# Kernel optimization log

Hardware: AMD Instinct MI355X
Metric: run time of the kernel (lower is better)

The kernel has to match this reference:

```python
import math
import jax, jax.numpy as jnp
import numpy as np

HEADS = 8
DIM = 512
HEAD_SIZE = DIM // HEADS  # 64


def setup_inputs() -> dict:
    key = jax.random.key(0)
    ks = jax.random.split(key, 5)
    b, nh, nw, t, d = 16, 16, 16, 16, DIM
    x = jax.random.normal(ks[0], (b, nh, nw, t, d), dtype=jnp.float32)
    s = 1.0 / math.sqrt(d)
    Wq = jax.random.normal(ks[1], (d, d), dtype=jnp.float32) * s
    Wk = jax.random.normal(ks[2], (d, d), dtype=jnp.float32) * s
    Wv = jax.random.normal(ks[3], (d, d), dtype=jnp.float32) * s
    Wo = jax.random.normal(ks[4], (d, d), dtype=jnp.float32) * s
    z = jnp.zeros((d,), dtype=jnp.float32)
    return {"x": x, "Wq": Wq, "bq": z, "Wk": Wk, "bk": z, "Wv": Wv, "bv": z, "Wo": Wo, "bo": z}


def _split_heads(t):
    # [b, n1, n2, T, D] -> [b, n1, n2, H, T, hs]
    b, n1, n2, T, _ = t.shape
    return t.reshape(b, n1, n2, T, HEADS, HEAD_SIZE).transpose(0, 1, 2, 4, 3, 5)


def reference(x, Wq, bq, Wk, bk, Wv, bv, Wo, bo):
    q = _split_heads(x @ Wq + bq)
    k = _split_heads(x @ Wk + bk)
    v = _split_heads(x @ Wv + bv)
    # windowed attention scores: [b, n1, n2, H, T, T]
    scores = jnp.einsum('bnmhtd,bnmhsd->bnmhts', q, k) / math.sqrt(HEAD_SIZE)
    probs = jax.nn.sigmoid(scores)  # NOTE: elementwise sigmoid, not softmax
    ctx = jnp.einsum('bnmhts,bnmhsd->bnmhtd', probs, v)
    b, n1, n2, H, T, hs = ctx.shape
    ctx = ctx.transpose(0, 1, 2, 4, 3, 5).reshape(b, n1, n2, T, H * hs)
    return ctx @ Wo + bo
```

## Files before the change

kernel.cpp:

```cpp
#include <hip/hip_runtime.h>
#include <hip/hip_bf16.h>

typedef float f32x4 __attribute__((ext_vector_type(4)));
typedef __bf16 bf16x8 __attribute__((ext_vector_type(8)));
typedef unsigned short u16x4 __attribute__((ext_vector_type(4)));
typedef unsigned short u16x8 __attribute__((ext_vector_type(8)));

__device__ __forceinline__ unsigned short f2bf(float f) {
  union { float f; unsigned u; } x; x.f = f;
  unsigned r = x.u + 0x7FFFu + ((x.u >> 16) & 1u);
  return (unsigned short)(r >> 16);
}

__device__ __forceinline__ void gl16(const void* g, void* l) {
  __builtin_amdgcn_global_load_lds(
      (const __attribute__((address_space(1))) unsigned*)g,
      (__attribute__((address_space(3))) unsigned*)l, 16, 0, 0);
}

__global__ __launch_bounds__(256) void prep_wt(const float* __restrict__ Wq,
                                               const float* __restrict__ Wk,
                                               const float* __restrict__ Wv,
                                               const float* __restrict__ Wo,
                                               unsigned short* __restrict__ WT) {
  __shared__ unsigned short ts[64][65];
  const float* W = (blockIdx.z == 0) ? Wq : (blockIdx.z == 1) ? Wk
                   : (blockIdx.z == 2) ? Wv : Wo;
  const int t = threadIdx.x;
  const int kbase = blockIdx.y * 64;
  const int nbase = blockIdx.x * 64;
  for (int i = 0; i < 16; ++i) {
    int idx = i * 256 + t;
    int r = idx >> 6, c = idx & 63;
    ts[r][c] = f2bf(W[(size_t)(kbase + r) * 512 + nbase + c]);
  }
  __syncthreads();
  unsigned short* dst = WT + (size_t)blockIdx.z * 512 * 512;
  for (int i = 0; i < 16; ++i) {
    int idx = i * 256 + t;
    int nn = idx >> 6, kk = idx & 63;
    dst[(size_t)(nbase + nn) * 512 + kbase + kk] = ts[kk][nn];
  }
}

__global__ void prep_bias(const float* __restrict__ bq, const float* __restrict__ bk,
                          const float* __restrict__ bv, float* __restrict__ biasc) {
  int i = blockIdx.x * 256 + threadIdx.x;
  if (i < 512) biasc[i] = bq[i];
  else if (i < 1024) biasc[i] = bk[i - 512];
  else if (i < 1536) biasc[i] = bv[i - 1024];
}

__global__ __launch_bounds__(256) void convert_x(const float* __restrict__ x,
                                                 unsigned short* __restrict__ xb,
                                                 long long n8) {
  long long i = (long long)blockIdx.x * 256 + threadIdx.x;
  const long long stride = (long long)gridDim.x * 256;
  for (; i < n8; i += stride) {
    f32x4 a = *reinterpret_cast<const f32x4*>(&x[i * 8]);
    f32x4 b = *reinterpret_cast<const f32x4*>(&x[i * 8 + 4]);
    u16x8 o;
    o[0] = f2bf(a[0]); o[1] = f2bf(a[1]); o[2] = f2bf(a[2]); o[3] = f2bf(a[3]);
    o[4] = f2bf(b[0]); o[5] = f2bf(b[1]); o[6] = f2bf(b[2]); o[7] = f2bf(b[3]);
    *reinterpret_cast<u16x8*>(&xb[i * 8]) = o;
  }
}

template <typename CT>
__global__ __launch_bounds__(512, 2) void gemm256(
    const unsigned short* __restrict__ A, int lda,
    const unsigned short* __restrict__ BT,
    CT* __restrict__ C, int ldc,
    const float* __restrict__ bias, int NB) {
  __shared__ alignas(16) unsigned short pool[66048];
  const int t = threadIdx.x;
  const int lane = t & 63;
  const int w = t >> 6;
  const int wm = w >> 2, wn = w & 3;

  const int nwg = gridDim.x;
  const int cpx = nwg >> 3;
  const int wg = (blockIdx.x & 7) * cpx + (blockIdx.x >> 3);
  const int n0 = (wg % NB) * 256;
  const int m0 = (wg / NB) * 256;

  const int sr = lane >> 3;
  const int sg = ((lane & 7) ^ sr) << 3;
  const unsigned short* gA = A + (size_t)(m0 + w * 8 + sr) * lda + sg;
  const unsigned short* gB = BT + (size_t)(n0 + w * 8 + sr) * 512 + sg;
  const int lw = w * 512;

#define STAGE_A(kt, h, b)                                                   \
  { const unsigned short* g_ = gA + (size_t)(h) * 128 * lda + (kt) * 64;    \
    unsigned short* l_ = &pool[(b) * 16384 + (h) * 8192 + lw];              \
    gl16(g_, l_); gl16(g_ + (size_t)64 * lda, l_ + 4096); }
#define STAGE_B(kt, h, b)                                                   \
  { const unsigned short* g_ = gB + (size_t)(h) * 128 * 512 + (kt) * 64;    \
    unsigned short* l_ = &pool[32768 + (b) * 16384 + (h) * 8192 + lw];      \
    gl16(g_, l_); gl16(g_ + (size_t)64 * 512, l_ + 4096); }

  const int fr = lane & 15;
  const int fg = lane >> 4;
  const int fx = lane & 7;
  auto readA = [&](int b, int mi, int kf) -> bf16x8 {
    return *reinterpret_cast<const bf16x8*>(
        &pool[(b) * 16384 + (wm * 128 + mi * 16 + fr) * 64 +
              ((((kf << 2) + fg) ^ fx) << 3)]);
  };
  auto readB = [&](int b, int ni, int kf) -> bf16x8 {
    return *reinterpret_cast<const bf16x8*>(
        &pool[32768 + (b) * 16384 + (wn * 64 + ni * 16 + fr) * 64 +
              ((((kf << 2) + fg) ^ fx) << 3)]);
  };

  f32x4 acc[8][4];
#pragma unroll
  for (int i = 0; i < 8; ++i)
#pragma unroll
    for (int j = 0; j < 4; ++j) acc[i][j] = (f32x4){0.f, 0.f, 0.f, 0.f};
  bf16x8 afr[8];
  bf16x8 bfr[4][2];

#define PHASE2(b, h, READB, STAGES, VM)                                      \
  {                                                                          \
    afr[0] = readA(b, 4 * (h) + 0, 0); afr[1] = readA(b, 4 * (h) + 0, 1);    \
    afr[2] = readA(b, 4 * (h) + 1, 0); afr[3] = readA(b, 4 * (h) + 1, 1);    \
    afr[4] = readA(b, 4 * (h) + 2, 0); afr[5] = readA(b, 4 * (h) + 2, 1);    \
    afr[6] = readA(b, 4 * (h) + 3, 0); afr[7] = readA(b, 4 * (h) + 3, 1);    \
    if (READB) {                                                             \
      _Pragma("unroll") for (int ni = 0; ni < 4; ++ni) {                     \
        bfr[ni][0] = readB(b, ni, 0);                                        \
        bfr[ni][1] = readB(b, ni, 1);                                        \
      }                                                                      \
    }                                                                        \
    STAGES;                                                                  \
    if ((VM) == 4) asm volatile("s_waitcnt vmcnt(4)" ::: "memory");          \
    if ((VM) == 0) asm volatile("s_waitcnt vmcnt(0)" ::: "memory");          \
    __builtin_amdgcn_s_barrier();                                            \
    asm volatile("s_waitcnt lgkmcnt(0)" ::: "memory");                       \
    __builtin_amdgcn_sched_barrier(0);                                       \
    __builtin_amdgcn_s_setprio(1);                                           \
    _Pragma("unroll") for (int ni = 0; ni < 4; ++ni)                         \
      _Pragma("unroll") for (int m4 = 0; m4 < 4; ++m4)                       \
        acc[4 * (h) + m4][ni] = __builtin_amdgcn_mfma_f32_16x16x32_bf16(     \
            afr[2 * m4], bfr[ni][0], acc[4 * (h) + m4][ni], 0, 0, 0);        \
    _Pragma("unroll") for (int ni = 0; ni < 4; ++ni)                         \
      _Pragma("unroll") for (int m4 = 0; m4 < 4; ++m4)                       \
        acc[4 * (h) + m4][ni] = __builtin_amdgcn_mfma_f32_16x16x32_bf16(     \
            afr[2 * m4 + 1], bfr[ni][1], acc[4 * (h) + m4][ni], 0, 0, 0);    \
    __builtin_amdgcn_s_setprio(0);                                           \
    __builtin_amdgcn_s_barrier();                                            \
  }

  STAGE_B(0, 0, 0); STAGE_B(0, 1, 0);
  STAGE_A(0, 0, 0); STAGE_A(0, 1, 0);
  STAGE_B(1, 0, 1); STAGE_B(1, 1, 1);
  asm volatile("s_waitcnt vmcnt(4)" ::: "memory");
  __builtin_amdgcn_s_barrier();

#pragma unroll
  for (int i = 0; i < 4; ++i) {
    const bool s2 = (i < 3);
    PHASE2(0, 0, true,  { STAGE_A(2 * i + 1, 0, 1) STAGE_A(2 * i + 1, 1, 1) }, -1);
    PHASE2(0, 1, false, { if (s2) { STAGE_B(2 * i + 2, 0, 0) STAGE_B(2 * i + 2, 1, 0) } }, s2 ? 4 : 0);
    PHASE2(1, 0, true,  { if (s2) { STAGE_A(2 * i + 2, 0, 0) STAGE_A(2 * i + 2, 1, 0) } }, -1);
    PHASE2(1, 1, false, { if (s2) { STAGE_B(2 * i + 3, 0, 1) STAGE_B(2 * i + 3, 1, 1) } }, s2 ? 4 : 0);
  }
#undef PHASE2
#undef STAGE_A
#undef STAGE_B

  __syncthreads();
  if constexpr (sizeof(CT) == 2) {
#pragma unroll
    for (int ni = 0; ni < 4; ++ni) {
      int cl = wn * 64 + ni * 16 + fr;
      float bc = bias[n0 + cl];
#pragma unroll
      for (int mi = 0; mi < 8; ++mi) {
        int rl = wm * 128 + mi * 16 + fg * 4;
#pragma unroll
        for (int r = 0; r < 4; ++r)
          pool[(rl + r) * 258 + cl] = f2bf(acc[mi][ni][r] + bc);
      }
    }
    __syncthreads();
#pragma unroll
    for (int it = 0; it < 16; ++it) {
      int idx = it * 512 + t;
      int row = idx >> 5, c8 = idx & 31;
      u16x8 v = *reinterpret_cast<const u16x8*>(&pool[row * 258 + c8 * 8]);
      *reinterpret_cast<u16x8*>(&C[(size_t)(m0 + row) * ldc + n0 + c8 * 8]) = v;
    }
  } else {
    float* stf = reinterpret_cast<float*>(pool);
#pragma unroll
    for (int h = 0; h < 2; ++h) {
      if (wm == h) {
#pragma unroll
        for (int ni = 0; ni < 4; ++ni) {
          int cl = wn * 64 + ni * 16 + fr;
          float bc = bias[n0 + cl];
#pragma unroll
          for (int mi = 0; mi < 8; ++mi) {
            int rl = mi * 16 + fg * 4;
#pragma unroll
            for (int r = 0; r < 4; ++r)
              stf[(rl + r) * 258 + cl] = acc[mi][ni][r] + bc;
          }
        }
      }
      __syncthreads();
#pragma unroll
      for (int it = 0; it < 16; ++it) {
        int idx = it * 512 + t;
        int row = idx >> 6, c4 = idx & 63;
        f32x4 v = *reinterpret_cast<const f32x4*>(&stf[row * 258 + c4 * 4]);
        *reinterpret_cast<f32x4*>(
            &C[(size_t)(m0 + h * 128 + row) * ldc + n0 + c4 * 4]) = v;
      }
      __syncthreads();
    }
  }
}

__global__ __launch_bounds__(256) void attn2(unsigned short* __restrict__ QKV) {
  __shared__ alignas(16) unsigned short sh[33792];
  const int VS = 16384, PS = 32768;
  const int t = threadIdx.x;
  const int lane = t & 63;
  const int w = t >> 6;
  const int fr = lane & 15, fg = lane >> 4, fx = lane & 7;
  const int sr = lane >> 3;
  const int sgx = ((lane & 7) ^ sr) << 3;
  const int sgl = (lane & 7) << 3;
  const size_t m0r = (size_t)blockIdx.x * 128;

#define SK2(h, b)                                                            \
  _Pragma("unroll") for (int u = 0; u < 4; ++u) {                            \
    const int r0 = u * 32 + w * 8;                                           \
    gl16(QKV + (m0r + r0 + sr) * 1536 + 512 + (h) * 64 + sgx,                \
         &sh[(b) * 8192 + r0 * 64]);                                         \
  }
#define SV2(h, b)                                                            \
  _Pragma("unroll") for (int u = 0; u < 4; ++u) {                            \
    const int r0 = u * 32 + w * 8;                                           \
    gl16(QKV + (m0r + r0 + sr) * 1536 + 1024 + (h) * 64 + sgl,               \
         &sh[VS + (b) * 8192 + r0 * 64]);                                    \
  }

  SK2(0, 0) SV2(0, 0)
  asm volatile("s_waitcnt vmcnt(0)" ::: "memory");
  __syncthreads();

  for (int h = 0; h < 8; ++h) {
    const int b = h & 1;
    u16x8 q[2][2];
#pragma unroll
    for (int ww = 0; ww < 2; ++ww) {
      const int wi = w * 2 + ww;
      const unsigned short* qrow = QKV + (m0r + wi * 16 + fr) * 1536 + h * 64;
      q[ww][0] = *reinterpret_cast<const u16x8*>(qrow + fg * 8);
      q[ww][1] = *reinterpret_cast<const u16x8*>(qrow + 32 + fg * 8);
    }
    if (h < 7) { SK2(h + 1, b ^ 1) SV2(h + 1, b ^ 1) }

#pragma unroll
    for (int ww = 0; ww < 2; ++ww) {
      const int wi = w * 2 + ww;
      f32x4 s = (f32x4){0.f, 0.f, 0.f, 0.f};
      {
        bf16x8 kf_ = *reinterpret_cast<const bf16x8*>(
            &sh[b * 8192 + (wi * 16 + fr) * 64 + ((fg ^ fx) << 3)]);
        s = __builtin_amdgcn_mfma_f32_16x16x32_bf16(
            kf_, __builtin_bit_cast(bf16x8, q[ww][0]), s, 0, 0, 0);
        kf_ = *reinterpret_cast<const bf16x8*>(
            &sh[b * 8192 + (wi * 16 + fr) * 64 + (((4 + fg) ^ fx) << 3)]);
        s = __builtin_amdgcn_mfma_f32_16x16x32_bf16(
            kf_, __builtin_bit_cast(bf16x8, q[ww][1]), s, 0, 0, 0);
      }
      u16x4 pfu;
#pragma unroll
      for (int r = 0; r < 4; ++r)
        pfu[r] = f2bf(1.0f / (1.0f + __expf(-s[r] * 0.125f)));
      *reinterpret_cast<u16x4*>(&sh[PS + w * 256 + fr * 16 + fg * 4]) = pfu;
      u16x8 pbu = (u16x8){0, 0, 0, 0, 0, 0, 0, 0};
      if (fg < 2)
        pbu = *reinterpret_cast<const u16x8*>(&sh[PS + w * 256 + fr * 16 + fg * 8]);
      bf16x8 pb = __builtin_bit_cast(bf16x8, pbu);
#pragma unroll
      for (int dc = 0; dc < 4; ++dc) {
        u16x8 vau;
#pragma unroll
        for (int j = 0; j < 8; ++j)
          vau[j] = sh[VS + b * 8192 + (wi * 16 + (fg & 1) * 8 + j) * 64 + dc * 16 + fr];
        f32x4 c = __builtin_amdgcn_mfma_f32_16x16x32_bf16(
            __builtin_bit_cast(bf16x8, vau), pb, (f32x4){0.f, 0.f, 0.f, 0.f},
            0, 0, 0);
        u16x4 o;
#pragma unroll
        for (int r = 0; r < 4; ++r) o[r] = f2bf(c[r]);
        *reinterpret_cast<u16x4*>(
            &QKV[(m0r + wi * 16 + fr) * 1536 + 1024 + h * 64 + dc * 16 + fg * 4]) = o;
      }
    }
    asm volatile("s_waitcnt vmcnt(8)" ::: "memory");
    __syncthreads();
  }
#undef SK2
#undef SV2
}

extern "C" void kernel_launch(void* const* d_in, const int* in_sizes, int n_in,
                              void* d_out, int out_size, void* d_ws, size_t ws_size,
                              hipStream_t stream) {
  const float* x  = (const float*)d_in[0];
  const float* Wq = (const float*)d_in[1];
  const float* bq = (const float*)d_in[2];
  const float* Wk = (const float*)d_in[3];
  const float* bk = (const float*)d_in[4];
  const float* Wv = (const float*)d_in[5];
  const float* bv = (const float*)d_in[6];
  const float* Wo = (const float*)d_in[7];
  const float* bo = (const float*)d_in[8];
  float* out = (float*)d_out;

  const int M = 65536;
  char* ws = (char*)d_ws;
  unsigned short* WT = (unsigned short*)ws;
  float* biasc = (float*)(ws + (size_t)2048 * 512 * 2);
  const long long prep_bytes = (long long)2048 * 512 * 2 + 8192;

  prep_wt<<<dim3(8, 8, 4), 256, 0, stream>>>(Wq, Wk, Wv, Wo, WT);
  prep_bias<<<6, 256, 0, stream>>>(bq, bk, bv, biasc);

  long long avail = (long long)ws_size - prep_bytes;
  int chunk_rows = 65536;
  while (chunk_rows > 2048 && (long long)chunk_rows * 4096 > avail) chunk_rows >>= 1;
  const int nchunks = M / chunk_rows;

  unsigned short* Xb  = (unsigned short*)(ws + prep_bytes);
  unsigned short* QKV = Xb + (size_t)chunk_rows * 512;

  for (int c = 0; c < nchunks; ++c) {
    const size_t row0 = (size_t)c * chunk_rows;
    const int mt = chunk_rows / 256;
    convert_x<<<2048, 256, 0, stream>>>(x + row0 * 512, Xb,
                                        (long long)chunk_rows * 64);
    gemm256<unsigned short><<<mt * 6, 512, 0, stream>>>(
        Xb, 512, WT, QKV, 1536, biasc, 6);
    attn2<<<chunk_rows / 128, 256, 0, stream>>>(QKV);
    gemm256<float><<<mt * 2, 512, 0, stream>>>(
        QKV + 1024, 1536, WT + (size_t)1536 * 512, out + row0 * 512, 512, bo, 2);
  }
}
```

Baseline: 294.3 us.

## Replace 256x256 GEMM tile with simpler 128x128 double-buffered kernel

Swaps the hand-pipelined 256x256, 512-thread GEMM for a 128x128-tile, 256-thread kernel with BK=32 and a plain two-buffer prefetch loop. The new kernel uses far less LDS and targets four workgroups per CU. The goal is higher occupancy and more workgroups to balance across CUs. In exchange, each tile reuses data less, so global and L2 traffic per FLOP goes up, and the finely interleaved load/MFMA schedule is dropped.

```diff
diff --git a/kernel.cpp b/kernel.cpp
--- a/kernel.cpp
+++ b/kernel.cpp
@@ -67,129 +67,100 @@
 }
 
 template <typename CT>
-__global__ __launch_bounds__(512, 2) void gemm256(
+__global__ __launch_bounds__(256, 4) void gemm128(
     const unsigned short* __restrict__ A, int lda,
     const unsigned short* __restrict__ BT,
     CT* __restrict__ C, int ldc,
     const float* __restrict__ bias, int NB) {
-  __shared__ alignas(16) unsigned short pool[66048];
+  __shared__ alignas(16) unsigned short pool[16640];
   const int t = threadIdx.x;
   const int lane = t & 63;
   const int w = t >> 6;
-  const int wm = w >> 2, wn = w & 3;
+  const int wm = w >> 1, wn = w & 1;
 
   const int nwg = gridDim.x;
   const int cpx = nwg >> 3;
   const int wg = (blockIdx.x & 7) * cpx + (blockIdx.x >> 3);
-  const int n0 = (wg % NB) * 256;
-  const int m0 = (wg / NB) * 256;
-
-  const int sr = lane >> 3;
-  const int sg = ((lane & 7) ^ sr) << 3;
-  const unsigned short* gA = A + (size_t)(m0 + w * 8 + sr) * lda + sg;
-  const unsigned short* gB = BT + (size_t)(n0 + w * 8 + sr) * 512 + sg;
-  const int lw = w * 512;
-
-#define STAGE_A(kt, h, b)                                                   \
-  { const unsigned short* g_ = gA + (size_t)(h) * 128 * lda + (kt) * 64;    \
-    unsigned short* l_ = &pool[(b) * 16384 + (h) * 8192 + lw];              \
-    gl16(g_, l_); gl16(g_ + (size_t)64 * lda, l_ + 4096); }
-#define STAGE_B(kt, h, b)                                                   \
-  { const unsigned short* g_ = gB + (size_t)(h) * 128 * 512 + (kt) * 64;    \
-    unsigned short* l_ = &pool[32768 + (b) * 16384 + (h) * 8192 + lw];      \
-    gl16(g_, l_); gl16(g_ + (size_t)64 * 512, l_ + 4096); }
+  const int n0 = (wg % NB) * 128;
+  const int m0 = (wg / NB) * 128;
+
+  const int sgr = lane >> 2;
+  const int sgc = ((lane & 3) ^ ((lane >> 3) & 3)) << 3;
+  const unsigned short* gA = A + (size_t)(m0 + w * 32 + sgr) * lda + sgc;
+  const unsigned short* gB = BT + (size_t)(n0 + w * 32 + sgr) * 512 + sgc;
+  const int lw = w * 1024;
+
+#define SA(kt, b)                                                           \
+  { const unsigned short* g_ = gA + (kt) * 32;                              \
+    gl16(g_, &pool[(b) * 4096 + lw]);                                       \
+    gl16(g_ + (size_t)16 * lda, &pool[(b) * 4096 + lw + 512]); }
+#define SB(kt, b)                                                           \
+  { const unsigned short* g_ = gB + (kt) * 32;                              \
+    gl16(g_, &pool[8192 + (b) * 4096 + lw]);                                \
+    gl16(g_ + (size_t)16 * 512, &pool[8192 + (b) * 4096 + lw + 512]); }
 
   const int fr = lane & 15;
   const int fg = lane >> 4;
-  const int fx = lane & 7;
-  auto readA = [&](int b, int mi, int kf) -> bf16x8 {
-    return *reinterpret_cast<const bf16x8*>(
-        &pool[(b) * 16384 + (wm * 128 + mi * 16 + fr) * 64 +
-              ((((kf << 2) + fg) ^ fx) << 3)]);
-  };
-  auto readB = [&](int b, int ni, int kf) -> bf16x8 {
-    return *reinterpret_cast<const bf16x8*>(
-        &pool[32768 + (b) * 16384 + (wn * 64 + ni * 16 + fr) * 64 +
-              ((((kf << 2) + fg) ^ fx) << 3)]);
-  };
-
-  f32x4 acc[8][4];
-#pragma unroll
-  for (int i = 0; i < 8; ++i)
+  const int aslot = (fg ^ ((fr >> 1) & 3)) << 3;
+
+  f32x4 acc[4][4];
+#pragma unroll
+  for (int i = 0; i < 4; ++i)
 #pragma unroll
     for (int j = 0; j < 4; ++j) acc[i][j] = (f32x4){0.f, 0.f, 0.f, 0.f};
-  bf16x8 afr[8];
-  bf16x8 bfr[4][2];
-
-#define PHASE2(b, h, READB, STAGES, VM)                                      \
-  {                                                                          \
-    afr[0] = readA(b, 4 * (h) + 0, 0); afr[1] = readA(b, 4 * (h) + 0, 1);    \
-    afr[2] = readA(b, 4 * (h) + 1, 0); afr[3] = readA(b, 4 * (h) + 1, 1);    \
-    afr[4] = readA(b, 4 * (h) + 2, 0); afr[5] = readA(b, 4 * (h) + 2, 1);    \
-    afr[6] = readA(b, 4 * (h) + 3, 0); afr[7] = readA(b, 4 * (h) + 3, 1);    \
-    if (READB) {                                                             \
-      _Pragma("unroll") for (int ni = 0; ni < 4; ++ni) {                     \
-        bfr[ni][0] = readB(b, ni, 0);                                        \
-        bfr[ni][1] = readB(b, ni, 1);                                        \
-      }                                                                      \
-    }                                                                        \
-    STAGES;                                                                  \
-    if ((VM) == 4) asm volatile("s_waitcnt vmcnt(4)" ::: "memory");          \
-    if ((VM) == 0) asm volatile("s_waitcnt vmcnt(0)" ::: "memory");          \
-    __builtin_amdgcn_s_barrier();                                            \
-    asm volatile("s_waitcnt lgkmcnt(0)" ::: "memory");                       \
-    __builtin_amdgcn_sched_barrier(0);                                       \
-    __builtin_amdgcn_s_setprio(1);                                           \
-    _Pragma("unroll") for (int ni = 0; ni < 4; ++ni)                         \
-      _Pragma("unroll") for (int m4 = 0; m4 < 4; ++m4)                       \
-        acc[4 * (h) + m4][ni] = __builtin_amdgcn_mfma_f32_16x16x32_bf16(     \
-            afr[2 * m4], bfr[ni][0], acc[4 * (h) + m4][ni], 0, 0, 0);        \
-    _Pragma("unroll") for (int ni = 0; ni < 4; ++ni)                         \
-      _Pragma("unroll") for (int m4 = 0; m4 < 4; ++m4)                       \
-        acc[4 * (h) + m4][ni] = __builtin_amdgcn_mfma_f32_16x16x32_bf16(     \
-            afr[2 * m4 + 1], bfr[ni][1], acc[4 * (h) + m4][ni], 0, 0, 0);    \
-    __builtin_amdgcn_s_setprio(0);                                           \
-    __builtin_amdgcn_s_barrier();                                            \
-  }
-
-  STAGE_B(0, 0, 0); STAGE_B(0, 1, 0);
-  STAGE_A(0, 0, 0); STAGE_A(0, 1, 0);
-  STAGE_B(1, 0, 1); STAGE_B(1, 1, 1);
-  asm volatile("s_waitcnt vmcnt(4)" ::: "memory");
+  bf16x8 afr[4], bfr[4];
+
+  SA(0, 0) SB(0, 0)
+  asm volatile("s_waitcnt vmcnt(0)" ::: "memory");
   __builtin_amdgcn_s_barrier();
 
 #pragma unroll
-  for (int i = 0; i < 4; ++i) {
-    const bool s2 = (i < 3);
-    PHASE2(0, 0, true,  { STAGE_A(2 * i + 1, 0, 1) STAGE_A(2 * i + 1, 1, 1) }, -1);
-    PHASE2(0, 1, false, { if (s2) { STAGE_B(2 * i + 2, 0, 0) STAGE_B(2 * i + 2, 1, 0) } }, s2 ? 4 : 0);
-    PHASE2(1, 0, true,  { if (s2) { STAGE_A(2 * i + 2, 0, 0) STAGE_A(2 * i + 2, 1, 0) } }, -1);
-    PHASE2(1, 1, false, { if (s2) { STAGE_B(2 * i + 3, 0, 1) STAGE_B(2 * i + 3, 1, 1) } }, s2 ? 4 : 0);
-  }
-#undef PHASE2
-#undef STAGE_A
-#undef STAGE_B
-
-  __syncthreads();
+  for (int kt = 0; kt < 16; ++kt) {
+    const int b = kt & 1;
+    if (kt < 15) { SA(kt + 1, b ^ 1) SB(kt + 1, b ^ 1) }
+#pragma unroll
+    for (int mi = 0; mi < 4; ++mi)
+      afr[mi] = *reinterpret_cast<const bf16x8*>(
+          &pool[b * 4096 + (wm * 64 + mi * 16 + fr) * 32 + aslot]);
+#pragma unroll
+    for (int ni = 0; ni < 4; ++ni)
+      bfr[ni] = *reinterpret_cast<const bf16x8*>(
+          &pool[8192 + b * 4096 + (wn * 64 + ni * 16 + fr) * 32 + aslot]);
+    asm volatile("s_waitcnt lgkmcnt(0)" ::: "memory");
+    __builtin_amdgcn_sched_barrier(0);
+    __builtin_amdgcn_s_setprio(1);
+#pragma unroll
+    for (int mi = 0; mi < 4; ++mi)
+#pragma unroll
+      for (int ni = 0; ni < 4; ++ni)
+        acc[mi][ni] = __builtin_amdgcn_mfma_f32_16x16x32_bf16(
+            afr[mi], bfr[ni], acc[mi][ni], 0, 0, 0);
+    __builtin_amdgcn_s_setprio(0);
+    asm volatile("s_waitcnt vmcnt(0)" ::: "memory");
+    __builtin_amdgcn_s_barrier();
+  }
+#undef SA
+#undef SB
+
   if constexpr (sizeof(CT) == 2) {
 #pragma unroll
     for (int ni = 0; ni < 4; ++ni) {
       int cl = wn * 64 + ni * 16 + fr;
       float bc = bias[n0 + cl];
 #pragma unroll
-      for (int mi = 0; mi < 8; ++mi) {
-        int rl = wm * 128 + mi * 16 + fg * 4;
+      for (int mi = 0; mi < 4; ++mi) {
+        int rl = wm * 64 + mi * 16 + fg * 4;
 #pragma unroll
         for (int r = 0; r < 4; ++r)
-          pool[(rl + r) * 258 + cl] = f2bf(acc[mi][ni][r] + bc);
+          pool[(rl + r) * 130 + cl] = f2bf(acc[mi][ni][r] + bc);
       }
     }
     __syncthreads();
 #pragma unroll
-    for (int it = 0; it < 16; ++it) {
-      int idx = it * 512 + t;
-      int row = idx >> 5, c8 = idx & 31;
-      u16x8 v = *reinterpret_cast<const u16x8*>(&pool[row * 258 + c8 * 8]);
+    for (int it = 0; it < 8; ++it) {
+      int idx = it * 256 + t;
+      int row = idx >> 4, c8 = idx & 15;
+      u16x8 v = *reinterpret_cast<const u16x8*>(&pool[row * 130 + c8 * 8]);
       *reinterpret_cast<u16x8*>(&C[(size_t)(m0 + row) * ldc + n0 + c8 * 8]) = v;
     }
   } else {
@@ -202,22 +173,22 @@
           int cl = wn * 64 + ni * 16 + fr;
           float bc = bias[n0 + cl];
 #pragma unroll
-          for (int mi = 0; mi < 8; ++mi) {
+          for (int mi = 0; mi < 4; ++mi) {
             int rl = mi * 16 + fg * 4;
 #pragma unroll
             for (int r = 0; r < 4; ++r)
-              stf[(rl + r) * 258 + cl] = acc[mi][ni][r] + bc;
+              stf[(rl + r) * 130 + cl] = acc[mi][ni][r] + bc;
           }
         }
       }
       __syncthreads();
 #pragma unroll
-      for (int it = 0; it < 16; ++it) {
-        int idx = it * 512 + t;
-        int row = idx >> 6, c4 = idx & 63;
-        f32x4 v = *reinterpret_cast<const f32x4*>(&stf[row * 258 + c4 * 4]);
+      for (int it = 0; it < 8; ++it) {
+        int idx = it * 256 + t;
+        int row = idx >> 5, c4 = idx & 31;
+        f32x4 v = *reinterpret_cast<const f32x4*>(&stf[row * 130 + c4 * 4]);
         *reinterpret_cast<f32x4*>(
-            &C[(size_t)(m0 + h * 128 + row) * ldc + n0 + c4 * 4]) = v;
+            &C[(size_t)(m0 + h * 64 + row) * ldc + n0 + c4 * 4]) = v;
       }
       __syncthreads();
     }
@@ -344,13 +315,13 @@
 
   for (int c = 0; c < nchunks; ++c) {
     const size_t row0 = (size_t)c * chunk_rows;
-    const int mt = chunk_rows / 256;
+    const int mt = chunk_rows / 128;
     convert_x<<<2048, 256, 0, stream>>>(x + row0 * 512, Xb,
                                         (long long)chunk_rows * 64);
-    gemm256<unsigned short><<<mt * 6, 512, 0, stream>>>(
-        Xb, 512, WT, QKV, 1536, biasc, 6);
+    gemm128<unsigned short><<<mt * 12, 256, 0, stream>>>(
+        Xb, 512, WT, QKV, 1536, biasc, 12);
     attn2<<<chunk_rows / 128, 256, 0, stream>>>(QKV);
-    gemm256<float><<<mt * 2, 512, 0, stream>>>(
-        QKV + 1024, 1536, WT + (size_t)1536 * 512, out + row0 * 512, 512, bo, 2);
-  }
-}
+    gemm128<float><<<mt * 4, 256, 0, stream>>>(
+        QKV + 1024, 1536, WT + (size_t)1536 * 512, out + row0 * 512, 512, bo, 4);
+  }
+}
```

New measurement: 294.2 us. Within noise of the previous version (-0.0%).
